# Performance work log

Measured on AMD Instinct MI355X. Metric: run time of the kernel, lower is better.

Reference implementation:

```python
import jax, jax.numpy as jnp
import numpy as np

N, M, D = 256, 1024, 512


def setup_inputs() -> dict:
    key = jax.random.key(0)
    ks = jax.random.split(key, 12)
    s = 1.0 / np.sqrt(D)
    return {
        "q": jax.random.normal(ks[0], (N, D), jnp.float32),
        "k": jax.random.normal(ks[1], (M, D), jnp.float32),
        "v": jax.random.normal(ks[2], (M, D), jnp.float32),
        "mask": jax.random.randint(ks[3], (N, M), 0, 2, jnp.int32),
        "WQ": jax.random.normal(ks[4], (D, D), jnp.float32) * s,
        "bQ": jax.random.normal(ks[5], (D,), jnp.float32) * s,
        "WK": jax.random.normal(ks[6], (D, D), jnp.float32) * s,
        "bK": jax.random.normal(ks[7], (D,), jnp.float32) * s,
        "WV": jax.random.normal(ks[8], (D, D), jnp.float32) * s,
        "bV": jax.random.normal(ks[9], (D,), jnp.float32) * s,
        "Ww": jax.random.normal(ks[10], (1, D), jnp.float32) * s,
        "bw": jax.random.normal(ks[11], (1,), jnp.float32) * s,
    }


def reference(q, k, v, mask, WQ, bQ, WK, bK, WV, bV, Ww, bw):
    # Linear projections (torch Linear: x @ W.T + b)
    qp = q @ WQ.T + bQ            # [N, D]
    kp = k @ WK.T + bK            # [M, D]
    vp = v @ WV.T + bV            # [M, D]
    # Additive (Bahdanau) scores: tanh(q_n + k_m) . w  -> [N, M]
    t = jnp.tanh(qp[:, None, :] + kp[None, :, :])   # [N, M, D]
    score = jnp.einsum("nmd,d->nm", t, Ww[0]) + bw[0]
    score = jnp.where(mask == 1, score, jnp.float32(-1e6))
    w = jax.nn.softmax(score, axis=1)               # softmax over keys (dim 1)
    context = jnp.einsum("nm,md->nd", w, vp)        # weighted sum over keys
    return context
```

## Files before the change

kernel.cpp:

```cpp
#include <hip/hip_runtime.h>

#define NQ 256
#define MK 1024
#define DD 512
#define CSC 2.8853900817779268f
#define L2E 1.4426950408889634f

typedef __attribute__((ext_vector_type(8))) short short8;
typedef __attribute__((ext_vector_type(4))) float floatx4;

__device__ inline int swz(int i, int d)
{
    return (((i >> 4) * 16 + (d >> 5)) << 9) | (((d >> 3) & 3) << 7)
         | ((i & 15) << 3) | (d & 7);
}

__device__ inline void bsplit(float x, unsigned short& h, unsigned short& l)
{
    unsigned u = __float_as_uint(x);
    unsigned hr = (u + 0x7FFFu + ((u >> 16) & 1u)) >> 16;
    h = (unsigned short)hr;
    float hf = __uint_as_float(hr << 16);
    unsigned ul = __float_as_uint(x - hf);
    l = (unsigned short)((ul + 0x7FFFu + ((ul >> 16) & 1u)) >> 16);
}

__global__ __launch_bounds__(256) void convert_split(
    const float* __restrict__ q, const float* __restrict__ k, const float* __restrict__ v,
    const float* __restrict__ WQ, const float* __restrict__ WK, const float* __restrict__ WV,
    unsigned short* __restrict__ qhi, unsigned short* __restrict__ qlo,
    unsigned short* __restrict__ khi, unsigned short* __restrict__ klo,
    unsigned short* __restrict__ vhi, unsigned short* __restrict__ vlo,
    unsigned short* __restrict__ wqhi, unsigned short* __restrict__ wqlo,
    unsigned short* __restrict__ wkhi, unsigned short* __restrict__ wklo,
    unsigned short* __restrict__ wvhi, unsigned short* __restrict__ wvlo)
{
    const int i4 = blockIdx.x * 256 + threadIdx.x;
    const float* src; unsigned short *dh, *dl; int li;
    if (i4 < 32768)       { src = q;  dh = qhi;  dl = qlo;  li = i4; }
    else if (i4 < 163840) { src = k;  dh = khi;  dl = klo;  li = i4 - 32768; }
    else if (i4 < 294912) { src = v;  dh = vhi;  dl = vlo;  li = i4 - 163840; }
    else if (i4 < 360448) { src = WQ; dh = wqhi; dl = wqlo; li = i4 - 294912; }
    else if (i4 < 425984) { src = WK; dh = wkhi; dl = wklo; li = i4 - 360448; }
    else                  { src = WV; dh = wvhi; dl = wvlo; li = i4 - 425984; }

    float4 x = *(const float4*)&src[li * 4];
    ushort4 h, l;
    bsplit(x.x, h.x, l.x); bsplit(x.y, h.y, l.y);
    bsplit(x.z, h.z, l.z); bsplit(x.w, h.w, l.w);

    const int e = li * 4;
    const int o = swz(e >> 9, e & 511);
    *(ushort4*)&dh[o] = h;
    *(ushort4*)&dl[o] = l;
}

__global__ __launch_bounds__(256) void proj_mfma(
    const unsigned short* __restrict__ qhi, const unsigned short* __restrict__ qlo,
    const unsigned short* __restrict__ khi, const unsigned short* __restrict__ klo,
    const unsigned short* __restrict__ vhi, const unsigned short* __restrict__ vlo,
    const unsigned short* __restrict__ wqhi, const unsigned short* __restrict__ wqlo,
    const unsigned short* __restrict__ wkhi, const unsigned short* __restrict__ wklo,
    const unsigned short* __restrict__ wvhi, const unsigned short* __restrict__ wvlo,
    const float* __restrict__ bQ, const float* __restrict__ bK, const float* __restrict__ bV,
    float* __restrict__ qe, float* __restrict__ ke, float* __restrict__ vp)
{
    int t = blockIdx.x;
    const unsigned short *Xh, *Xl, *Wh, *Wl; const float* b; int mode;
    if (t < 32)       { mode = 0; Xh = qhi; Xl = qlo; Wh = wqhi; Wl = wqlo; b = bQ; }
    else if (t < 160) { mode = 1; t -= 32;  Xh = khi; Xl = klo; Wh = wkhi; Wl = wklo; b = bK; }
    else              { mode = 2; t -= 160; Xh = vhi; Xl = vlo; Wh = wvhi; Wl = wvlo; b = bV; }
    const int i0 = (t >> 3) * 64;
    const int j0 = (t & 7) * 64;

    const int l  = threadIdx.x & 63;
    const int w  = threadIdx.x >> 6;
    const int lr = l & 15;
    const int rbase = (l >> 4) * 4;

    const unsigned short* Ah = Xh + ((i0 >> 4) + w) * 8192 + l * 8;
    const unsigned short* Al = Xl + ((i0 >> 4) + w) * 8192 + l * 8;
    const unsigned short* Bh = Wh + (j0 >> 4) * 8192 + l * 8;
    const unsigned short* Bl = Wl + (j0 >> 4) * 8192 + l * 8;

    floatx4 acc[4] = {{0,0,0,0},{0,0,0,0},{0,0,0,0},{0,0,0,0}};

#pragma unroll
    for (int kc = 0; kc < 16; ++kc) {
        short8 ah = *(const short8*)(Ah + kc * 512);
        short8 al = *(const short8*)(Al + kc * 512);
#pragma unroll
        for (int nt = 0; nt < 4; ++nt) {
            short8 bh = *(const short8*)(Bh + nt * 8192 + kc * 512);
            short8 bl = *(const short8*)(Bl + nt * 8192 + kc * 512);
            acc[nt] = __builtin_amdgcn_mfma_f32_16x16x32_bf16(ah, bh, acc[nt], 0, 0, 0);
            acc[nt] = __builtin_amdgcn_mfma_f32_16x16x32_bf16(ah, bl, acc[nt], 0, 0, 0);
            acc[nt] = __builtin_amdgcn_mfma_f32_16x16x32_bf16(al, bh, acc[nt], 0, 0, 0);
        }
    }

    if (mode == 1) {
#pragma unroll
        for (int nt = 0; nt < 4; ++nt) {
            const int d = j0 + nt * 16 + lr;
            const float bb = b[d];
            float* base = &ke[(((d >> 3) * MK) + i0 + w * 16 + rbase) * 8 + (d & 7)];
#pragma unroll
            for (int j = 0; j < 4; ++j)
                base[j * 8] = __builtin_amdgcn_exp2f((acc[nt][j] + bb) * CSC);
        }
    } else {
        float* dst = (mode == 0) ? qe : vp;
#pragma unroll
        for (int nt = 0; nt < 4; ++nt) {
            const float bb = b[j0 + nt * 16 + lr];
#pragma unroll
            for (int j = 0; j < 4; ++j) {
                float val = acc[nt][j] + bb;
                if (mode == 0) val = __builtin_amdgcn_exp2f(val * CSC);
                dst[(i0 + w * 16 + rbase + j) * DD + j0 + nt * 16 + lr] = val;
            }
        }
    }
}

__global__ __launch_bounds__(1024) void score_sm(
    const float* __restrict__ qe, const float* __restrict__ kts,
    const float* __restrict__ Ww, const int* __restrict__ mask,
    float* __restrict__ S)
{
    const int n = blockIdx.x;
    const int t = threadIdx.x;
    const int lane = t & 63, wave = t >> 6;

    __shared__ float qw[DD * 2];
    __shared__ float red[16];

    if (t < DD) { qw[t * 2] = qe[n * DD + t]; qw[t * 2 + 1] = Ww[t]; }
    __syncthreads();

    const float* kp = kts + t * 8;
    float acc = 0.f;
    float4 k0 = *(const float4*)(kp);
    float4 k1 = *(const float4*)(kp + 4);
    for (int c = 0; c < 64; ++c) {
        float4 p0 = k0, p1 = k1;
        if (c + 1 < 64) {
            p0 = *(const float4*)(kp + (c + 1) * (MK * 8));
            p1 = *(const float4*)(kp + (c + 1) * (MK * 8) + 4);
        }
        float kv[8] = {k0.x, k0.y, k0.z, k0.w, k1.x, k1.y, k1.z, k1.w};
#pragma unroll
        for (int j = 0; j < 8; j += 2) {
            float4 qq = *(const float4*)&qw[(c * 8 + j) * 2];
            float e0 = qq.x * kv[j];
            float e1 = qq.z * kv[j + 1];
            acc = fmaf(qq.y, __builtin_amdgcn_rcpf(e0 + 1.0f), acc);
            acc = fmaf(qq.w, __builtin_amdgcn_rcpf(e1 + 1.0f), acc);
        }
        k0 = p0; k1 = p1;
    }

    float s = -2.0f * acc;
    s = (mask[n * MK + t] == 1) ? s : -1e6f;

    float mx = s;
    for (int o = 32; o > 0; o >>= 1) mx = fmaxf(mx, __shfl_xor(mx, o, 64));
    if (lane == 0) red[wave] = mx;
    __syncthreads();
    if (wave == 0) {
        float r = red[lane & 15];
        for (int o = 8; o > 0; o >>= 1) r = fmaxf(r, __shfl_xor(r, o, 64));
        if (lane == 0) red[0] = r;
    }
    __syncthreads();
    mx = red[0];
    __syncthreads();

    float e = __builtin_amdgcn_exp2f((s - mx) * L2E);
    float sum = e;
    for (int o = 32; o > 0; o >>= 1) sum += __shfl_xor(sum, o, 64);
    if (lane == 0) red[wave] = sum;
    __syncthreads();
    if (wave == 0) {
        float r = red[lane & 15];
        for (int o = 8; o > 0; o >>= 1) r += __shfl_xor(r, o, 64);
        if (lane == 0) red[0] = r;
    }
    __syncthreads();
    sum = red[0];

    S[n * MK + t] = e * __builtin_amdgcn_rcpf(sum);
}

#define XNG 4

__global__ __launch_bounds__(512) void context_v3(const float* __restrict__ S,
                                                  const float* __restrict__ vp,
                                                  float* __restrict__ out)
{
    __shared__ float ws[MK][XNG];
    __shared__ float pacc[4][XNG][128];
    const int t = threadIdx.x;
    const int n0 = blockIdx.x * XNG;
    const int d0 = blockIdx.y * 128;

#pragma unroll
    for (int p = 0; p < 8; ++p) {
        int e = t + p * 512;
        int nn = e >> 10, m = e & 1023;
        ws[m][nn] = S[(n0 + nn) * MK + m];
    }
    __syncthreads();

    const int d = d0 + (t & 127);
    const int seg = t >> 7;
    float acc[XNG] = {};
    for (int m = seg * 256; m < seg * 256 + 256; ++m) {
        float vv = vp[m * DD + d];
        float4 w = *(const float4*)&ws[m][0];
        acc[0] = fmaf(w.x, vv, acc[0]);
        acc[1] = fmaf(w.y, vv, acc[1]);
        acc[2] = fmaf(w.z, vv, acc[2]);
        acc[3] = fmaf(w.w, vv, acc[3]);
    }
#pragma unroll
    for (int nn = 0; nn < XNG; ++nn) pacc[seg][nn][t & 127] = acc[nn];
    __syncthreads();

    if (t < XNG * 128) {
        int nn = t >> 7, dd = t & 127;
        float r = pacc[0][nn][dd] + pacc[1][nn][dd]
                + pacc[2][nn][dd] + pacc[3][nn][dd];
        out[(n0 + nn) * DD + d0 + dd] = r;
    }
}

extern "C" void kernel_launch(void* const* d_in, const int* in_sizes, int n_in,
                              void* d_out, int out_size, void* d_ws, size_t ws_size,
                              hipStream_t stream)
{
    const float* q    = (const float*)d_in[0];
    const float* k    = (const float*)d_in[1];
    const float* v    = (const float*)d_in[2];
    const int*   mask = (const int*)  d_in[3];
    const float* WQ   = (const float*)d_in[4];
    const float* bQ   = (const float*)d_in[5];
    const float* WK   = (const float*)d_in[6];
    const float* bK   = (const float*)d_in[7];
    const float* WV   = (const float*)d_in[8];
    const float* bV   = (const float*)d_in[9];
    const float* Ww   = (const float*)d_in[10];
    const float* bw   = (const float*)d_in[11];
    (void)bw;
    float* out = (float*)d_out;

    float* qe  = (float*)d_ws;
    float* ke  = qe + NQ * DD;
    float* vp  = ke + DD * MK;
    float* S   = vp + MK * DD;
    unsigned short* p16  = (unsigned short*)(S + NQ * MK);
    unsigned short* qhi  = p16;              p16 += NQ * DD;
    unsigned short* qlo  = p16;              p16 += NQ * DD;
    unsigned short* khi  = p16;              p16 += MK * DD;
    unsigned short* klo  = p16;              p16 += MK * DD;
    unsigned short* vhi  = p16;              p16 += MK * DD;
    unsigned short* vlo  = p16;              p16 += MK * DD;
    unsigned short* wqhi = p16;              p16 += DD * DD;
    unsigned short* wqlo = p16;              p16 += DD * DD;
    unsigned short* wkhi = p16;              p16 += DD * DD;
    unsigned short* wklo = p16;              p16 += DD * DD;
    unsigned short* wvhi = p16;              p16 += DD * DD;
    unsigned short* wvlo = p16;

    convert_split<<<1920, 256, 0, stream>>>(q, k, v, WQ, WK, WV,
        qhi, qlo, khi, klo, vhi, vlo, wqhi, wqlo, wkhi, wklo, wvhi, wvlo);

    proj_mfma<<<288, 256, 0, stream>>>(qhi, qlo, khi, klo, vhi, vlo,
        wqhi, wqlo, wkhi, wklo, wvhi, wvlo, bQ, bK, bV, qe, ke, vp);

    score_sm<<<NQ, 1024, 0, stream>>>(qe, ke, Ww, mask, S);

    context_v3<<<dim3(NQ / XNG, 4), 512, 0, stream>>>(S, vp, out);
}
```

Measured before the change: 144.7 us.

## Split score kernel into multi-query tiled score pass and separate softmax

The score kernel now has each thread compute four query rows against one key, so every key load is reused four times. The D dimension is split across two wave groups and the partial sums are combined in shared memory. The grid changes to 4x64 blocks of 512 threads instead of 256 blocks of 1024. Softmax moves to a separate 256-thread kernel, which adds a launch and an extra round trip of S through global memory in exchange for less key traffic. Query and weight values are now read from global/cache via uniform loads rather than from shared memory.

```diff
diff --git a/kernel.cpp b/kernel.cpp
--- a/kernel.cpp
+++ b/kernel.cpp
@@ -124,73 +124,98 @@
     }
 }
 
-__global__ __launch_bounds__(1024) void score_sm(
-    const float* __restrict__ qe, const float* __restrict__ kts,
+#define SN 4
+
+__global__ __launch_bounds__(512) void score_v4(
+    const float* __restrict__ qe, const float* __restrict__ ke,
     const float* __restrict__ Ww, const int* __restrict__ mask,
     float* __restrict__ S)
+{
+    const int t = threadIdx.x;
+    const int lane = t & 63;
+    const int w = t >> 6;
+    const int mg = w & 3;
+    const int dh = __builtin_amdgcn_readfirstlane(w >> 2);
+    const int m0 = blockIdx.x * 256;
+    const int m  = m0 + mg * 64 + lane;
+    const int n0 = blockIdx.y * SN;
+
+    __shared__ float part[2][SN][256];
+
+    const float* qb = qe + n0 * DD + dh * 256;
+    const float* wb = Ww + dh * 256;
+    const float* kb = ke + (size_t)(dh * 32) * (MK * 8) + m * 8;
+
+    float acc[SN] = {0.f, 0.f, 0.f, 0.f};
+    float4 k0 = *(const float4*)(kb);
+    float4 k1 = *(const float4*)(kb + 4);
+    for (int c = 0; c < 32; ++c) {
+        float4 p0 = k0, p1 = k1;
+        if (c + 1 < 32) {
+            p0 = *(const float4*)(kb + (c + 1) * (MK * 8));
+            p1 = *(const float4*)(kb + (c + 1) * (MK * 8) + 4);
+        }
+        float kv[8] = {k0.x, k0.y, k0.z, k0.w, k1.x, k1.y, k1.z, k1.w};
+#pragma unroll
+        for (int j = 0; j < 8; ++j) {
+            const float ww = wb[c * 8 + j];
+#pragma unroll
+            for (int n = 0; n < SN; ++n) {
+                float e = fmaf(qb[n * DD + c * 8 + j], kv[j], 1.0f);
+                acc[n] = fmaf(ww, __builtin_amdgcn_rcpf(e), acc[n]);
+            }
+        }
+        k0 = p0; k1 = p1;
+    }
+
+#pragma unroll
+    for (int n = 0; n < SN; ++n) part[dh][n][mg * 64 + lane] = acc[n];
+    __syncthreads();
+
+    if (w < 4) {
+#pragma unroll
+        for (int n = 0; n < SN; ++n) {
+            float s = -2.0f * (part[0][n][mg * 64 + lane] + part[1][n][mg * 64 + lane]);
+            s = (mask[(n0 + n) * MK + m] == 1) ? s : -1e6f;
+            S[(n0 + n) * MK + m] = s;
+        }
+    }
+}
+
+__global__ __launch_bounds__(256) void softmax_kernel(float* __restrict__ S)
 {
     const int n = blockIdx.x;
     const int t = threadIdx.x;
     const int lane = t & 63, wave = t >> 6;
-
-    __shared__ float qw[DD * 2];
-    __shared__ float red[16];
-
-    if (t < DD) { qw[t * 2] = qe[n * DD + t]; qw[t * 2 + 1] = Ww[t]; }
-    __syncthreads();
-
-    const float* kp = kts + t * 8;
-    float acc = 0.f;
-    float4 k0 = *(const float4*)(kp);
-    float4 k1 = *(const float4*)(kp + 4);
-    for (int c = 0; c < 64; ++c) {
-        float4 p0 = k0, p1 = k1;
-        if (c + 1 < 64) {
-            p0 = *(const float4*)(kp + (c + 1) * (MK * 8));
-            p1 = *(const float4*)(kp + (c + 1) * (MK * 8) + 4);
-        }
-        float kv[8] = {k0.x, k0.y, k0.z, k0.w, k1.x, k1.y, k1.z, k1.w};
-#pragma unroll
-        for (int j = 0; j < 8; j += 2) {
-            float4 qq = *(const float4*)&qw[(c * 8 + j) * 2];
-            float e0 = qq.x * kv[j];
-            float e1 = qq.z * kv[j + 1];
-            acc = fmaf(qq.y, __builtin_amdgcn_rcpf(e0 + 1.0f), acc);
-            acc = fmaf(qq.w, __builtin_amdgcn_rcpf(e1 + 1.0f), acc);
-        }
-        k0 = p0; k1 = p1;
-    }
-
-    float s = -2.0f * acc;
-    s = (mask[n * MK + t] == 1) ? s : -1e6f;
-
-    float mx = s;
+    __shared__ float red[4];
+
+    float v[4];
+    float mx = -3.4e38f;
+#pragma unroll
+    for (int i = 0; i < 4; ++i) {
+        v[i] = S[n * MK + t + i * 256];
+        mx = fmaxf(mx, v[i]);
+    }
     for (int o = 32; o > 0; o >>= 1) mx = fmaxf(mx, __shfl_xor(mx, o, 64));
     if (lane == 0) red[wave] = mx;
     __syncthreads();
-    if (wave == 0) {
-        float r = red[lane & 15];
-        for (int o = 8; o > 0; o >>= 1) r = fmaxf(r, __shfl_xor(r, o, 64));
-        if (lane == 0) red[0] = r;
-    }
-    __syncthreads();
-    mx = red[0];
-    __syncthreads();
-
-    float e = __builtin_amdgcn_exp2f((s - mx) * L2E);
-    float sum = e;
+    mx = fmaxf(fmaxf(red[0], red[1]), fmaxf(red[2], red[3]));
+    __syncthreads();
+
+    float sum = 0.f;
+#pragma unroll
+    for (int i = 0; i < 4; ++i) {
+        v[i] = __builtin_amdgcn_exp2f((v[i] - mx) * L2E);
+        sum += v[i];
+    }
     for (int o = 32; o > 0; o >>= 1) sum += __shfl_xor(sum, o, 64);
     if (lane == 0) red[wave] = sum;
     __syncthreads();
-    if (wave == 0) {
-        float r = red[lane & 15];
-        for (int o = 8; o > 0; o >>= 1) r += __shfl_xor(r, o, 64);
-        if (lane == 0) red[0] = r;
-    }
-    __syncthreads();
-    sum = red[0];
-
-    S[n * MK + t] = e * __builtin_amdgcn_rcpf(sum);
+    sum = red[0] + red[1] + red[2] + red[3];
+
+    const float inv = __builtin_amdgcn_rcpf(sum);
+#pragma unroll
+    for (int i = 0; i < 4; ++i) S[n * MK + t + i * 256] = v[i] * inv;
 }
 
 #define XNG 4
@@ -279,7 +304,9 @@
     proj_mfma<<<288, 256, 0, stream>>>(qhi, qlo, khi, klo, vhi, vlo,
         wqhi, wqlo, wkhi, wklo, wvhi, wvlo, bQ, bK, bV, qe, ke, vp);
 
-    score_sm<<<NQ, 1024, 0, stream>>>(qe, ke, Ww, mask, S);
+    score_v4<<<dim3(4, NQ / SN), 512, 0, stream>>>(qe, ke, Ww, mask, S);
+
+    softmax_kernel<<<NQ, 256, 0, stream>>>(S);
 
     context_v3<<<dim3(NQ / XNG, 4), 512, 0, stream>>>(S, vp, out);
 }
```

Result: no change. 144.3 us (-0.2%).
